# Performance work log

Hardware: AMD Instinct MI355X
Metric: run time of the kernel (lower is better)

Reference implementation:

```python
import jax, jax.numpy as jnp
import numpy as np

T, B, I, H = 512, 64, 1024, 1024


def setup_inputs() -> dict:
    key = jax.random.key(0)
    ks = jax.random.split(key, 9)
    g_x = 1.0 / np.sqrt(I)   # glorot-ish scale
    g_h = 1.0 / np.sqrt(H)
    return {
        "X": jax.random.normal(ks[0], (T, B, I), dtype=jnp.float32),
        "Wa_x": jax.random.normal(ks[1], (I, H), dtype=jnp.float32) * g_x,
        "Wi_x": jax.random.normal(ks[2], (I, H), dtype=jnp.float32) * g_x,
        "Wf_x": jax.random.normal(ks[3], (I, H), dtype=jnp.float32) * g_x,
        "Wo_x": jax.random.normal(ks[4], (I, H), dtype=jnp.float32) * g_x,
        "Wa_h": jax.random.normal(ks[5], (H, H), dtype=jnp.float32) * g_h,
        "Wi_h": jax.random.normal(ks[6], (H, H), dtype=jnp.float32) * g_h,
        "Wf_h": jax.random.normal(ks[7], (H, H), dtype=jnp.float32) * g_h,
        "Wo_h": jax.random.normal(ks[8], (H, H), dtype=jnp.float32) * g_h,
        "ba": jnp.zeros((H,), dtype=jnp.float32),
        "bi": jnp.zeros((H,), dtype=jnp.float32),
        "bf": jnp.zeros((H,), dtype=jnp.float32),
        "bo": jnp.zeros((H,), dtype=jnp.float32),
    }


def reference(X, Wa_x, Wi_x, Wf_x, Wo_x, Wa_h, Wi_h, Wf_h, Wo_h, ba, bi, bf, bo):
    # Fuse the 4 input-to-gate GEMMs across all timesteps (no recurrence there):
    # Xg: [T, B, 4H] with gate order (a, i, f, o)
    Wx = jnp.concatenate([Wa_x, Wi_x, Wf_x, Wo_x], axis=1)  # [I, 4H]
    Wh = jnp.concatenate([Wa_h, Wi_h, Wf_h, Wo_h], axis=1)  # [H, 4H]
    b = jnp.concatenate([ba, bi, bf, bo], axis=0)           # [4H]
    Xg = jnp.einsum("tbi,ig->tbg", X, Wx) + b               # [T, B, 4H]

    Hd = Wa_h.shape[0]

    def step(carry, xg):
        h, s = carry
        g = xg + h @ Wh  # [B, 4H]; at t=0, h=0 so matches the t==0 branch
        a = jnp.tanh(g[:, 0 * Hd:1 * Hd])
        i = jax.nn.sigmoid(g[:, 1 * Hd:2 * Hd])
        f = jax.nn.sigmoid(g[:, 2 * Hd:3 * Hd])
        o = jax.nn.sigmoid(g[:, 3 * Hd:4 * Hd])
        s_new = a * i + s * f
        h_new = jnp.tanh(s_new) * o
        return (h_new, s_new), h_new

    Bsz = X.shape[1]
    init = (jnp.zeros((Bsz, Hd), X.dtype), jnp.zeros((Bsz, Hd), X.dtype))
    _, outputs = jax.lax.scan(step, init, Xg)  # [T, B, H]
    return outputs


if __name__ == "__main__":
    out = reference(**setup_inputs())
    print(out.shape)
```

## Files before the change

### kernel.cpp

```cpp
#include <hip/hip_runtime.h>
#include <hip/hip_bf16.h>

typedef __bf16 bf8 __attribute__((ext_vector_type(8)));
typedef float  f32x4  __attribute__((ext_vector_type(4)));
typedef float  f32x16 __attribute__((ext_vector_type(16)));
typedef unsigned long long u64;

#define TT 512
#define BBATCH 64
#define IDIM 1024
#define HDIM 1024
#define G4 4096
#define NREC 128

__device__ __forceinline__ float sigf(float x) {
  x = fminf(fmaxf(x, -30.f), 30.f);
  return 1.f / (1.f + __expf(-x));
}
__device__ __forceinline__ float tanh_(float x) {
  x = fminf(fmaxf(x, -15.f), 15.f);
  float e = __expf(2.f * x);
  return (e - 1.f) / (e + 1.f);
}
__device__ __forceinline__ f32x4 MFMA(bf8 a, bf8 b, f32x4 c) {
  return __builtin_amdgcn_mfma_f32_16x16x32_bf16(a, b, c, 0, 0, 0);
}
__device__ __forceinline__ f32x16 MFMA32(bf8 a, bf8 b, f32x16 c) {
  return __builtin_amdgcn_mfma_f32_32x32x16_bf16(a, b, c, 0, 0, 0);
}

__global__ __launch_bounds__(256) void k_convw(
    const float* __restrict__ s0, const float* __restrict__ s1,
    const float* __restrict__ s2, const float* __restrict__ s3,
    const float* __restrict__ s4, const float* __restrict__ s5,
    const float* __restrict__ s6, const float* __restrict__ s7,
    __bf16* __restrict__ WxT, __bf16* __restrict__ WhT) {
  int z = blockIdx.z;
  const float* src = (z == 0) ? s0 : (z == 1) ? s1 : (z == 2) ? s2 :
                     (z == 3) ? s3 : (z == 4) ? s4 : (z == 5) ? s5 :
                     (z == 6) ? s6 : s7;
  __bf16* dst = (z < 4) ? WxT : WhT;
  int j0 = blockIdx.x * 64, k0 = blockIdx.y * 64;
  __shared__ float T[64][65];
  int tid = threadIdx.x;
#pragma unroll
  for (int i = 0; i < 16; ++i) {
    int idx = tid + i * 256;
    int kl = idx >> 6, jl = idx & 63;
    T[kl][jl] = src[(size_t)(k0 + kl) * 1024 + j0 + jl];
  }
  __syncthreads();
#pragma unroll
  for (int i = 0; i < 2; ++i) {
    int Gt = tid + i * 256;
    int nl = Gt >> 3, gq = Gt & 7;
    int n = (z & 3) * 1024 + j0 + nl;
    bf8 v;
#pragma unroll
    for (int e = 0; e < 8; ++e) v[e] = (__bf16)T[gq * 8 + e][nl];
    *(bf8*)&dst[(size_t)n * 1024 + k0 + gq * 8] = v;
  }
}

__global__ void k_bias(const float* __restrict__ b0, const float* __restrict__ b1,
                       const float* __restrict__ b2, const float* __restrict__ b3,
                       float* __restrict__ bias) {
  int i = blockIdx.x * 256 + threadIdx.x;
  if (i < G4) {
    const float* s = (i < 1024) ? b0 : (i < 2048) ? b1 : (i < 3072) ? b2 : b3;
    bias[i] = s[i & 1023];
  }
}

__global__ __launch_bounds__(512, 1) void k_fused(
    const float* __restrict__ Xg_r, float* __restrict__ Xg_w,
    const __bf16* __restrict__ WhT, const __bf16* __restrict__ WxT,
    const float* __restrict__ Xnext, const float* __restrict__ bias,
    __bf16* __restrict__ hb0, __bf16* __restrict__ hb1,
    float* __restrict__ S, float* __restrict__ out,
    int* flags, int t0, int Tc, int nrec, int gM) {
  __shared__ char smem[65536];
  const int bid = blockIdx.x, tid = threadIdx.x;
  const int lane = tid & 63, w = tid >> 6;

  if (bid < nrec) {
    bf8 (*Ls)[128] = (bf8(*)[128])smem;
    float* Gsf = (float*)smem;
    const int nc = w & 1, kq = w >> 1;
    const int rh = bid & 1, hc0 = (bid >> 1) * 16;
    const int l31 = lane & 31, hi = lane >> 5;
    const int rowbase = rh * 32;

    bf8 Bf[16];
    {
      const int lc = nc * 32 + l31;
      const __bf16* wp = WhT + (size_t)((lc >> 4) * 1024 + hc0 + (lc & 15)) * 1024 +
                         kq * 256 + hi * 8;
#pragma unroll
      for (int s = 0; s < 16; ++s) Bf[s] = *(const bf8*)(wp + s * 16);
    }
#pragma unroll
    for (int i = 0; i < 16; ++i) {
      float4 tp = __builtin_bit_cast(float4, Bf[i]);
      asm volatile("" : "+v"(tp.x), "+v"(tp.y), "+v"(tp.z), "+v"(tp.w));
      Bf[i] = __builtin_bit_cast(bf8, tp);
    }

    const int er = tid >> 4, ec = tid & 15;
    float sreg = 0.f;
    if (t0 > 0) sreg = S[(size_t)(rowbase + er) * 1024 + hc0 + ec];

    for (int lt = 0; lt < Tc; ++lt) {
      const int t = t0 + lt;

      const float* xp = Xg_r + ((size_t)lt * 64 + rowbase + er) * G4 + hc0 + ec;
      float xa = xp[0], xi = xp[1024], xf = xp[2048], xo = xp[3072];

      if (t > 0) {
        if (lt > 0) {
          int v;
          do {
            v = __hip_atomic_load(flags + (2 * lane + rh) * 32, __ATOMIC_RELAXED,
                                  __HIP_MEMORY_SCOPE_AGENT);
          } while (!__all(v >= t));
          asm volatile("" ::: "memory");
        }
        const __bf16* hp = ((t - 1) & 1) ? hb1 : hb0;

        union { u64 q[2]; bf8 v; } vv[8];
#pragma unroll
        for (int i = 0; i < 8; ++i) {
          int g = i * 512 + tid;
          const u64* sp = (const u64*)(hp + (size_t)(rowbase + (g >> 7)) * 1024 +
                                       (g & 127) * 8);
          vv[i].q[0] = __hip_atomic_load((u64*)sp, __ATOMIC_RELAXED,
                                         __HIP_MEMORY_SCOPE_AGENT);
          vv[i].q[1] = __hip_atomic_load((u64*)sp + 1, __ATOMIC_RELAXED,
                                         __HIP_MEMORY_SCOPE_AGENT);
        }
#pragma unroll
        for (int i = 0; i < 8; ++i) {
          int g = i * 512 + tid, r = g >> 7, cg = g & 127;
          Ls[r][cg ^ (r & 7)] = vv[i].v;
        }
        __syncthreads();

        f32x16 acc = {};
#pragma unroll
        for (int s = 0; s < 16; ++s) {
          int c = (kq * 16 + s) * 2 + hi;
          bf8 af = Ls[l31][c ^ (l31 & 7)];
          acc = MFMA32(af, Bf[s], acc);
        }
        __syncthreads();

        {
          float* gt = Gsf + (nc * 4 + kq) * 1024 + l31 * 32;
#pragma unroll
          for (int q = 0; q < 4; ++q) {
            int rg = 2 * q + hi;
            f32x4 v4 = { acc[4 * q + 0], acc[4 * q + 1],
                         acc[4 * q + 2], acc[4 * q + 3] };
            *(f32x4*)(gt + ((rg ^ (l31 & 7)) << 2)) = v4;
          }
        }
        __syncthreads();

        {
          const int rg = er >> 2, e = er & 3;
#pragma unroll
          for (int g = 0; g < 4; ++g) {
            int lc2 = g * 16 + ec;
            int ncl = lc2 >> 5, col = lc2 & 31;
            const float* gp = Gsf + ncl * 4096 + col * 32 +
                              ((rg ^ (col & 7)) << 2) + e;
            float v = gp[0] + gp[1024] + gp[2048] + gp[3072];
            if (g == 0) xa += v;
            else if (g == 1) xi += v;
            else if (g == 2) xf += v;
            else xo += v;
          }
        }
      }

      float av = tanh_(xa), iv = sigf(xi), fv = sigf(xf), ov = sigf(xo);
      sreg = av * iv + sreg * fv;
      float h0 = tanh_(sreg) * ov;

      out[((size_t)t * 64 + rowbase + er) * 1024 + hc0 + ec] = h0;

      float hnb = __shfl(h0, lane + 1);
      if ((ec & 1) == 0) {
        unsigned int pv =
            (unsigned int)__builtin_bit_cast(unsigned short, (__bf16)h0) |
            ((unsigned int)__builtin_bit_cast(unsigned short, (__bf16)hnb) << 16);
        __bf16* hn = (t & 1) ? hb1 : hb0;
        __hip_atomic_store(
            (unsigned int*)((char*)hn + ((size_t)(rowbase + er) * 1024 + hc0 + ec) * 2),
            pv, __ATOMIC_RELAXED, __HIP_MEMORY_SCOPE_AGENT);
      }

      __syncthreads();
      if (tid == 0)
        __hip_atomic_store(flags + bid * 32, t + 1, __ATOMIC_RELAXED,
                           __HIP_MEMORY_SCOPE_AGENT);
    }

    S[(size_t)(rowbase + er) * 1024 + hc0 + ec] = sreg;
    return;
  }

  if (gM == 0) return;
  const int nw = gridDim.x - nrec;
  const int wid = bid - nrec;
  __bf16 (*As)[40] = (__bf16(*)[40])smem;
  __bf16 (*Bs)[40] = (__bf16(*)[40])(smem + 128 * 40 * 2);
  const int wr = (w >> 2) * 64, wc = (w & 3) * 32;
  const int sm = tid >> 2, sk = (tid & 3) * 8;
  const int gl15 = lane & 15, glq = lane >> 4;
  const int ntiles = (gM / 128) * (G4 / 128);

  for (int tile = wid; tile < ntiles; tile += nw) {
    const int m0 = (tile >> 5) * 128, n0 = (tile & 31) * 128;
    const float*  Ap = Xnext + (size_t)(m0 + sm) * 1024 + sk;
    const __bf16* Bp = WxT + (size_t)(n0 + sm) * 1024 + sk;
    f32x4 acc[4][2] = {};
    float4 ra0, ra1;
    bf8 rb;
    auto ld = [&](int kt) {
      ra0 = *(const float4*)(Ap + kt * 32);
      ra1 = *(const float4*)(Ap + kt * 32 + 4);
      rb = *(const bf8*)(Bp + kt * 32);
    };
    ld(0);
    for (int kt = 0; kt < 32; ++kt) {
      __syncthreads();
      bf8 va;
      va[0]=(__bf16)ra0.x; va[1]=(__bf16)ra0.y; va[2]=(__bf16)ra0.z; va[3]=(__bf16)ra0.w;
      va[4]=(__bf16)ra1.x; va[5]=(__bf16)ra1.y; va[6]=(__bf16)ra1.z; va[7]=(__bf16)ra1.w;
      *(bf8*)&As[sm][sk] = va;
      *(bf8*)&Bs[sm][sk] = rb;
      if (kt < 31) ld(kt + 1);
      __syncthreads();
      bf8 af[4], bv[2];
#pragma unroll
      for (int r = 0; r < 4; ++r) af[r] = *(const bf8*)&As[wr + r * 16 + gl15][glq * 8];
#pragma unroll
      for (int c = 0; c < 2; ++c) bv[c] = *(const bf8*)&Bs[wc + c * 16 + gl15][glq * 8];
#pragma unroll
      for (int r = 0; r < 4; ++r)
#pragma unroll
        for (int c = 0; c < 2; ++c)
          acc[r][c] = MFMA(af[r], bv[c], acc[r][c]);
    }
#pragma unroll
    for (int c = 0; c < 2; ++c) {
      int col = n0 + wc + c * 16 + gl15;
      float bc = bias[col];
#pragma unroll
      for (int r = 0; r < 4; ++r)
#pragma unroll
        for (int q = 0; q < 4; ++q)
          Xg_w[(size_t)(m0 + wr + r * 16 + glq * 4 + q) * G4 + col] = acc[r][c][q] + bc;
    }
    __syncthreads();
  }
}

extern "C" void kernel_launch(void* const* d_in, const int* in_sizes, int n_in,
                              void* d_out, int out_size, void* d_ws, size_t ws_size,
                              hipStream_t stream) {
  const float* X  = (const float*)d_in[0];
  const float* wa = (const float*)d_in[1];
  const float* wi = (const float*)d_in[2];
  const float* wf = (const float*)d_in[3];
  const float* wo = (const float*)d_in[4];
  const float* ha = (const float*)d_in[5];
  const float* hi = (const float*)d_in[6];
  const float* hf = (const float*)d_in[7];
  const float* ho = (const float*)d_in[8];
  const float* b0 = (const float*)d_in[9];
  const float* b1 = (const float*)d_in[10];
  const float* b2 = (const float*)d_in[11];
  const float* b3 = (const float*)d_in[12];
  float* out = (float*)d_out;
  char* ws = (char*)d_ws;

  size_t off = 0;
  auto alloc = [&](size_t bytes) {
    void* p = ws + off;
    off += (bytes + 255) & ~(size_t)255;
    return p;
  };
  __bf16* WxT = (__bf16*)alloc((size_t)G4 * IDIM * 2);
  __bf16* WhT = (__bf16*)alloc((size_t)G4 * HDIM * 2);
  float* bias = (float*)alloc(G4 * 4);
  float* S    = (float*)alloc((size_t)BBATCH * HDIM * 4);
  __bf16* hb0 = (__bf16*)alloc((size_t)BBATCH * HDIM * 2);
  __bf16* hb1 = (__bf16*)alloc((size_t)BBATCH * HDIM * 2);
  int* flags  = (int*)alloc(NREC * 32 * 4);
  size_t base = off;

  const size_t perXg = (size_t)BBATCH * G4 * 4;
  int Tc = 64;
  while (Tc > 4 && base + 2 * (size_t)Tc * perXg > ws_size) Tc >>= 1;
  float* Xg0 = (float*)(ws + base);
  float* Xg1 = (float*)(ws + base + (size_t)Tc * perXg);
  int nchunks = TT / Tc;

  k_convw<<<dim3(16, 16, 8), dim3(256), 0, stream>>>(wa, wi, wf, wo, ha, hi, hf,
                                                     ho, WxT, WhT);
  k_bias<<<dim3(16), dim3(256), 0, stream>>>(b0, b1, b2, b3, bias);
  hipMemsetAsync(flags, 0, NREC * 32 * 4, stream);

  k_fused<<<dim3(256), dim3(512), 0, stream>>>(
      nullptr, Xg0, WhT, WxT, X, bias, hb0, hb1, S, out, flags,
      0, 0, 0, Tc * BBATCH);

  for (int c = 0; c < nchunks; ++c) {
    float* xr = (c & 1) ? Xg1 : Xg0;
    float* xw = (c & 1) ? Xg0 : Xg1;
    int gM = (c + 1 < nchunks) ? Tc * BBATCH : 0;
    const float* Xn = X + (size_t)(c + 1) * Tc * BBATCH * IDIM;
    k_fused<<<dim3(256), dim3(512), 0, stream>>>(
        xr, xw, WhT, WxT, Xn, bias, hb0, hb1, S, out, flags,
        c * Tc, Tc, NREC, gM);
  }
}
```

Before: 2.109 ms.

## Store h in MFMA fragment layout and load A operands directly into registers

The hidden state buffer is now written in a pre-swizzled layout that matches the MFMA A-fragment order, so each wave loads its A operands straight from global memory into registers. This removes the LDS staging of h and one barrier per step. Each wave now owns a 128-wide K slice across both N columns (two accumulators) instead of a 256-wide slice for one column. The K-split partials are reduced in two passes through LDS: an 8-way sum, then the gate gather. This trades the LDS write and read of h for more redundant global loads per wave and an extra reduction stage.

```diff
diff --git a/kernel.cpp b/kernel.cpp
--- a/kernel.cpp
+++ b/kernel.cpp
@@ -84,31 +84,35 @@
   const int lane = tid & 63, w = tid >> 6;
 
   if (bid < nrec) {
-    bf8 (*Ls)[128] = (bf8(*)[128])smem;
     float* Gsf = (float*)smem;
-    const int nc = w & 1, kq = w >> 1;
+    const int ko = w;
     const int rh = bid & 1, hc0 = (bid >> 1) * 16;
     const int l31 = lane & 31, hi = lane >> 5;
     const int rowbase = rh * 32;
 
-    bf8 Bf[16];
-    {
+    bf8 Bf[2][8];
+#pragma unroll
+    for (int nc = 0; nc < 2; ++nc) {
       const int lc = nc * 32 + l31;
       const __bf16* wp = WhT + (size_t)((lc >> 4) * 1024 + hc0 + (lc & 15)) * 1024 +
-                         kq * 256 + hi * 8;
-#pragma unroll
-      for (int s = 0; s < 16; ++s) Bf[s] = *(const bf8*)(wp + s * 16);
+                         ko * 128 + hi * 8;
+#pragma unroll
+      for (int s = 0; s < 8; ++s) Bf[nc][s] = *(const bf8*)(wp + s * 16);
     }
 #pragma unroll
-    for (int i = 0; i < 16; ++i) {
-      float4 tp = __builtin_bit_cast(float4, Bf[i]);
-      asm volatile("" : "+v"(tp.x), "+v"(tp.y), "+v"(tp.z), "+v"(tp.w));
-      Bf[i] = __builtin_bit_cast(bf8, tp);
-    }
+    for (int nc = 0; nc < 2; ++nc)
+#pragma unroll
+      for (int i = 0; i < 8; ++i) {
+        float4 tp = __builtin_bit_cast(float4, Bf[nc][i]);
+        asm volatile("" : "+v"(tp.x), "+v"(tp.y), "+v"(tp.z), "+v"(tp.w));
+        Bf[nc][i] = __builtin_bit_cast(bf8, tp);
+      }
 
     const int er = tid >> 4, ec = tid & 15;
     float sreg = 0.f;
     if (t0 > 0) sreg = S[(size_t)(rowbase + er) * 1024 + hc0 + ec];
+
+    const size_t hoff = ((size_t)((hc0 >> 3) + (ec >> 3)) * 32 + er) * 8 + (ec & 6);
 
     for (int lt = 0; lt < Tc; ++lt) {
       const int t = t0 + lt;
@@ -125,61 +129,63 @@
           } while (!__all(v >= t));
           asm volatile("" ::: "memory");
         }
-        const __bf16* hp = ((t - 1) & 1) ? hb1 : hb0;
-
-        union { u64 q[2]; bf8 v; } vv[8];
-#pragma unroll
-        for (int i = 0; i < 8; ++i) {
-          int g = i * 512 + tid;
-          const u64* sp = (const u64*)(hp + (size_t)(rowbase + (g >> 7)) * 1024 +
-                                       (g & 127) * 8);
-          vv[i].q[0] = __hip_atomic_load((u64*)sp, __ATOMIC_RELAXED,
-                                         __HIP_MEMORY_SCOPE_AGENT);
-          vv[i].q[1] = __hip_atomic_load((u64*)sp + 1, __ATOMIC_RELAXED,
-                                         __HIP_MEMORY_SCOPE_AGENT);
+        const __bf16* hA = (((t - 1) & 1) ? hb1 : hb0) + (size_t)rh * 32768;
+
+        const u64* ap = (const u64*)(hA + ((size_t)(ko * 16 + hi) * 32 + l31) * 8);
+        union { u64 q[2]; bf8 v; } a0, a1, a2, a3, a4, a5, a6, a7;
+#define LD_A(AV, S) \
+        AV.q[0] = __hip_atomic_load(ap + (S) * 128, __ATOMIC_RELAXED, \
+                                    __HIP_MEMORY_SCOPE_AGENT); \
+        AV.q[1] = __hip_atomic_load(ap + (S) * 128 + 1, __ATOMIC_RELAXED, \
+                                    __HIP_MEMORY_SCOPE_AGENT);
+        LD_A(a0, 0) LD_A(a1, 1) LD_A(a2, 2) LD_A(a3, 3)
+        LD_A(a4, 4) LD_A(a5, 5) LD_A(a6, 6) LD_A(a7, 7)
+#undef LD_A
+
+        f32x16 acc0 = {}, acc1 = {};
+#define MM(AV, S) \
+        acc0 = MFMA32(AV.v, Bf[0][S], acc0); \
+        acc1 = MFMA32(AV.v, Bf[1][S], acc1);
+        MM(a0, 0) MM(a1, 1) MM(a2, 2) MM(a3, 3)
+        MM(a4, 4) MM(a5, 5) MM(a6, 6) MM(a7, 7)
+#undef MM
+
+#pragma unroll
+        for (int q = 0; q < 4; ++q) {
+          const int rg = 2 * q + hi;
+          const int off = l31 * 32 + ((rg ^ (l31 & 7)) << 2);
+          f32x4 v0 = { acc0[4 * q + 0], acc0[4 * q + 1],
+                       acc0[4 * q + 2], acc0[4 * q + 3] };
+          f32x4 v1 = { acc1[4 * q + 0], acc1[4 * q + 1],
+                       acc1[4 * q + 2], acc1[4 * q + 3] };
+          *(f32x4*)&Gsf[(0 * 8 + ko) * 1024 + off] = v0;
+          *(f32x4*)&Gsf[(1 * 8 + ko) * 1024 + off] = v1;
         }
-#pragma unroll
-        for (int i = 0; i < 8; ++i) {
-          int g = i * 512 + tid, r = g >> 7, cg = g & 127;
-          Ls[r][cg ^ (r & 7)] = vv[i].v;
-        }
-        __syncthreads();
-
-        f32x16 acc = {};
-#pragma unroll
-        for (int s = 0; s < 16; ++s) {
-          int c = (kq * 16 + s) * 2 + hi;
-          bf8 af = Ls[l31][c ^ (l31 & 7)];
-          acc = MFMA32(af, Bf[s], acc);
-        }
-        __syncthreads();
-
-        {
-          float* gt = Gsf + (nc * 4 + kq) * 1024 + l31 * 32;
-#pragma unroll
-          for (int q = 0; q < 4; ++q) {
-            int rg = 2 * q + hi;
-            f32x4 v4 = { acc[4 * q + 0], acc[4 * q + 1],
-                         acc[4 * q + 2], acc[4 * q + 3] };
-            *(f32x4*)(gt + ((rg ^ (l31 & 7)) << 2)) = v4;
-          }
-        }
-        __syncthreads();
-
-        {
-          const int rg = er >> 2, e = er & 3;
-#pragma unroll
-          for (int g = 0; g < 4; ++g) {
-            int lc2 = g * 16 + ec;
-            int ncl = lc2 >> 5, col = lc2 & 31;
-            const float* gp = Gsf + ncl * 4096 + col * 32 +
-                              ((rg ^ (col & 7)) << 2) + e;
-            float v = gp[0] + gp[1024] + gp[2048] + gp[3072];
-            if (g == 0) xa += v;
-            else if (g == 1) xi += v;
-            else if (g == 2) xf += v;
-            else xo += v;
-          }
+      }
+      __syncthreads();
+
+      if (t > 0) {
+        const int tt = tid >> 8, col = (tid >> 3) & 31, rg = tid & 7;
+        const int off = col * 32 + ((rg ^ (col & 7)) << 2);
+        f32x4 sum = *(const f32x4*)&Gsf[tt * 8192 + off];
+#pragma unroll
+        for (int k2 = 1; k2 < 8; ++k2)
+          sum += *(const f32x4*)&Gsf[tt * 8192 + k2 * 1024 + off];
+        *(f32x4*)&Gsf[tt * 8192 + off] = sum;
+      }
+      __syncthreads();
+
+      if (t > 0) {
+        const int rg2 = er >> 2, e = er & 3;
+#pragma unroll
+        for (int g = 0; g < 4; ++g) {
+          const int lc2 = g * 16 + ec;
+          const int tt2 = lc2 >> 5, col2 = lc2 & 31;
+          float v = Gsf[tt2 * 8192 + col2 * 32 + ((rg2 ^ (col2 & 7)) << 2) + e];
+          if (g == 0) xa += v;
+          else if (g == 1) xi += v;
+          else if (g == 2) xf += v;
+          else xo += v;
         }
       }
 
@@ -194,10 +200,9 @@
         unsigned int pv =
             (unsigned int)__builtin_bit_cast(unsigned short, (__bf16)h0) |
             ((unsigned int)__builtin_bit_cast(unsigned short, (__bf16)hnb) << 16);
-        __bf16* hn = (t & 1) ? hb1 : hb0;
-        __hip_atomic_store(
-            (unsigned int*)((char*)hn + ((size_t)(rowbase + er) * 1024 + hc0 + ec) * 2),
-            pv, __ATOMIC_RELAXED, __HIP_MEMORY_SCOPE_AGENT);
+        __bf16* hAn = ((t & 1) ? hb1 : hb0) + (size_t)rh * 32768;
+        __hip_atomic_store((unsigned int*)((char*)hAn + hoff * 2), pv,
+                           __ATOMIC_RELAXED, __HIP_MEMORY_SCOPE_AGENT);
       }
 
       __syncthreads();
```

New measurement: 2.032 ms. 1.04x faster.
